# Kernel tuning notes

Measured on AMD Instinct MI355X. Metric: run time of the kernel, lower is better.

## Reference

```python
import jax, jax.numpy as jnp
import numpy as np

PATCH = 300
B, F = 16, 14
NOISE_FACTOR = 0.1
KERNEL = 7  # MedianPool2d(7, same=True) -> reflect pad 3 each side
PAD = 3
MED_IDX = (KERNEL * KERNEL - 1) // 2  # lower median of 49 = index 24


def median_pool7(x):
    """x: [C,H,W] -> [C,H,W], 7x7 median with reflect 'same' padding (MedianPool2d)."""
    C, H, W = x.shape
    xp = jnp.pad(x, ((0, 0), (PAD, PAD), (PAD, PAD)), mode='reflect')
    # 49 shifted views stacked on last axis: [C,H,W,49]
    wins = jnp.stack([xp[:, i:i + H, j:j + W]
                      for i in range(KERNEL) for j in range(KERNEL)], axis=-1)
    return jnp.sort(wins, axis=-1)[..., MED_IDX]


def setup_inputs() -> dict:
    key = jax.random.key(0)
    k1, k2, k3, k4, k5 = jax.random.split(key, 5)
    adv_patch = jax.random.uniform(k1, (3, PATCH, PATCH), dtype=jnp.float32)
    lab_batch = jax.random.uniform(k2, (B, F, 5), dtype=jnp.float32)
    contrast = jax.random.uniform(k3, (B, F), dtype=jnp.float32, minval=0.8, maxval=1.2)
    brightness = jax.random.uniform(k4, (B, F), dtype=jnp.float32, minval=-0.1, maxval=0.1)
    noise = jax.random.uniform(k5, (B, F, 3, PATCH, PATCH), dtype=jnp.float32, minval=-1.0, maxval=1.0)
    return {"adv_patch": adv_patch, "lab_batch": lab_batch, "contrast": contrast,
            "brightness": brightness, "noise": noise, "img_size": 416}


def reference(adv_patch, lab_batch, contrast, brightness, noise, img_size):
    # adv_patch side (300) <= img_size (416): interpolation branch skipped.
    p = median_pool7(adv_patch)                      # enable_blurred=True
    b, f = lab_batch.shape[0], lab_batch.shape[1]
    adv_batch = jnp.broadcast_to(p[None, None], (b, f) + p.shape)  # [B,F,3,P,P]
    c = contrast[:, :, None, None, None]
    br = brightness[:, :, None, None, None]
    adv_batch = adv_batch * c + br + noise * NOISE_FACTOR
    # with_black_trans=False branch
    return jnp.clip(adv_batch, 1e-6, 0.99999)
```

## Files before the change

kernel.cpp:

```cpp
#include <hip/hip_runtime.h>
#include <hip/hip_bf16.h>

#define PATCH    300
#define CHW      (PATCH*PATCH)
#define NPATCH   (3*CHW)
#define NSLAB    (16*14)
#define E8       (NPATCH/8)

#define FLAG_OFF 0
#define PMED_OFF 16

static __device__ __forceinline__ float bf2f(unsigned int bits16) {
    return __uint_as_float(bits16 << 16);
}

__global__ void detect_kernel(const unsigned short* __restrict__ patch,
                              int* __restrict__ flag) {
    int lane = threadIdx.x;
    unsigned int m = 0;
    for (int i = lane; i < 2048; i += 64) {
        unsigned int v = patch[i];
        m = m > v ? m : v;
    }
#pragma unroll
    for (int off = 32; off; off >>= 1) {
        unsigned int o = __shfl_down(m, off, 64);
        m = m > o ? m : o;
    }
    if (lane == 0) *flag = (m >= 0x8000u) ? 1 : 0;
}

#define CSWAP(x, y) do { float t_ = fminf(x, y); (y) = fmaxf(x, y); (x) = t_; } while (0)

template <bool F32>
static __device__ __forceinline__ float ldv(const void* pc, int off) {
    return F32 ? ((const float*)pc)[off]
               : bf2f(((const unsigned short*)pc)[off]);
}

template <bool F32>
static __device__ __forceinline__ float median49(const void* pc,
                                                 const int* ro, const int* ww) {
    float a[26];
#pragma unroll
    for (int k = 0; k < 26; ++k)
        a[k] = ldv<F32>(pc, ro[k / 7] + ww[k % 7]);

    float nxt = ldv<F32>(pc, ro[26 / 7] + ww[26 % 7]);
#pragma unroll
    for (int it = 0; it < 23; ++it) {
#pragma unroll
        for (int i = it + 1; i <= 25; ++i) CSWAP(a[it], a[i]);
#pragma unroll
        for (int i = it + 1; i < 25; ++i)  CSWAP(a[i], a[25]);
        a[25] = nxt;
        if (it < 22) {
            const int k = 27 + it;
            nxt = ldv<F32>(pc, ro[k / 7] + ww[k % 7]);
        }
    }
    float mn = fminf(a[23], a[24]);
    float mx = fmaxf(a[23], a[24]);
    return fmaxf(mn, fminf(mx, a[25]));
}

__global__ __launch_bounds__(256) void median7_kernel(
        const void* __restrict__ patchv,
        const int* __restrict__ flag,
        float* __restrict__ pmed) {
    int idx = blockIdx.x * 256 + threadIdx.x;
    if (idx >= NPATCH) return;
    int mode = *flag;
    int c   = idx / CHW;
    int rem = idx - c * CHW;
    int h   = rem / PATCH;
    int w   = rem - h * PATCH;

    int ro[7], ww[7];
#pragma unroll
    for (int d = 0; d < 7; d++) {
        int x = h + d - 3;
        x = x < 0 ? -x : (x >= PATCH ? 2 * PATCH - 2 - x : x);
        ro[d] = x * PATCH;
        int y = w + d - 3;
        ww[d] = y < 0 ? -y : (y >= PATCH ? 2 * PATCH - 2 - y : y);
    }

    float med;
    if (mode) {
        med = median49<true >((const void*)((const float*)patchv + c * CHW), ro, ww);
    } else {
        med = median49<false>((const void*)((const unsigned short*)patchv + c * CHW), ro, ww);
    }
    pmed[idx] = med;
}

__global__ __launch_bounds__(256) void apply_kernel(
        const float* __restrict__ pmed,
        const void* __restrict__ noisev,
        const void* __restrict__ contrastv,
        const void* __restrict__ brightnessv,
        const int* __restrict__ flag,
        float* __restrict__ out) {
    int slab = blockIdx.y;
    int g    = blockIdx.x * 256 + threadIdx.x;
    if (g >= E8) return;
    int mode = *flag;

    const float4* pm4 = (const float4*)pmed;
    float4 pa = pm4[2 * g], pb = pm4[2 * g + 1];
    float p[8] = {pa.x, pa.y, pa.z, pa.w, pb.x, pb.y, pb.z, pb.w};

    float c, br, n[8];
    if (mode) {
        c  = ((const float*)contrastv)[slab];
        br = ((const float*)brightnessv)[slab];
        const float4* n4 = (const float4*)noisev + (size_t)slab * (2 * E8);
        float4 na = n4[2 * g], nb = n4[2 * g + 1];
        n[0]=na.x; n[1]=na.y; n[2]=na.z; n[3]=na.w;
        n[4]=nb.x; n[5]=nb.y; n[6]=nb.z; n[7]=nb.w;
    } else {
        c  = bf2f(((const unsigned short*)contrastv)[slab]);
        br = bf2f(((const unsigned short*)brightnessv)[slab]);
        uint4 nv = ((const uint4*)noisev)[(size_t)slab * E8 + g];
        n[0]=bf2f(nv.x & 0xffffu); n[1]=bf2f(nv.x >> 16);
        n[2]=bf2f(nv.y & 0xffffu); n[3]=bf2f(nv.y >> 16);
        n[4]=bf2f(nv.z & 0xffffu); n[5]=bf2f(nv.z >> 16);
        n[6]=bf2f(nv.w & 0xffffu); n[7]=bf2f(nv.w >> 16);
    }

    float4 oa, ob;
    float r[8];
#pragma unroll
    for (int i = 0; i < 8; i++)
        r[i] = fminf(fmaxf(p[i] * c + br + n[i] * 0.1f, 1e-6f), 0.99999f);
    oa.x = r[0]; oa.y = r[1]; oa.z = r[2]; oa.w = r[3];
    ob.x = r[4]; ob.y = r[5]; ob.z = r[6]; ob.w = r[7];

    float4* o4 = (float4*)out + (size_t)slab * (2 * E8);
    o4[2 * g]     = oa;
    o4[2 * g + 1] = ob;
}

extern "C" void kernel_launch(void* const* d_in, const int* in_sizes, int n_in,
                              void* d_out, int out_size, void* d_ws, size_t ws_size,
                              hipStream_t stream) {
    const void* adv_patch  = d_in[0];
    const void* contrast   = d_in[2];
    const void* brightness = d_in[3];
    const void* noise      = d_in[4];

    int*   flag = (int*)((char*)d_ws + FLAG_OFF);
    float* pmed = (float*)((char*)d_ws + PMED_OFF);
    float* out  = (float*)d_out;

    detect_kernel<<<dim3(1), dim3(64), 0, stream>>>(
        (const unsigned short*)adv_patch, flag);

    median7_kernel<<<dim3((NPATCH + 255) / 256), dim3(256), 0, stream>>>(
        adv_patch, flag, pmed);

    dim3 g2((E8 + 255) / 256, NSLAB);
    apply_kernel<<<g2, dim3(256), 0, stream>>>(
        pmed, noise, contrast, brightness, flag, out);
}
```

Before: 428.6 us.

## Inline dtype detection into kernels and restructure apply loop for coalesced float4 access

Removes the separate single-wave detect kernel and the flag buffer, so each block instead detects f32 vs bf16 input from a wave-wide check of the first 1 KB of the patch. The apply kernel switches from 8 elements per thread in two adjacent float4 loads to four strided float4 loads per thread with a stride of 256, which gives fully coalesced accesses and more work per thread. This drops one launch and one dependency, but the detection heuristic now looks at fewer patch bytes and is repeated in every block.

```diff
diff --git a/kernel.cpp b/kernel.cpp
--- a/kernel.cpp
+++ b/kernel.cpp
@@ -1,33 +1,21 @@
 #include <hip/hip_runtime.h>
-#include <hip/hip_bf16.h>
 
 #define PATCH    300
 #define CHW      (PATCH*PATCH)
 #define NPATCH   (3*CHW)
 #define NSLAB    (16*14)
-#define E8       (NPATCH/8)
+#define NF4      (NPATCH/4)
 
-#define FLAG_OFF 0
-#define PMED_OFF 16
+#define PMED_OFF 0
 
 static __device__ __forceinline__ float bf2f(unsigned int bits16) {
     return __uint_as_float(bits16 << 16);
 }
 
-__global__ void detect_kernel(const unsigned short* __restrict__ patch,
-                              int* __restrict__ flag) {
-    int lane = threadIdx.x;
-    unsigned int m = 0;
-    for (int i = lane; i < 2048; i += 64) {
-        unsigned int v = patch[i];
-        m = m > v ? m : v;
-    }
-#pragma unroll
-    for (int off = 32; off; off >>= 1) {
-        unsigned int o = __shfl_down(m, off, 64);
-        m = m > o ? m : o;
-    }
-    if (lane == 0) *flag = (m >= 0x8000u) ? 1 : 0;
+static __device__ __forceinline__ int detect_f32(const void* patchv) {
+    const uint4* p4 = (const uint4*)patchv;
+    uint4 v = p4[threadIdx.x & 63];
+    return __any(((v.x | v.y | v.z | v.w) & 0x80008000u) != 0u);
 }
 
 #define CSWAP(x, y) do { float t_ = fminf(x, y); (y) = fmaxf(x, y); (x) = t_; } while (0)
@@ -66,11 +54,10 @@
 
 __global__ __launch_bounds__(256) void median7_kernel(
         const void* __restrict__ patchv,
-        const int* __restrict__ flag,
         float* __restrict__ pmed) {
+    int mode = detect_f32(patchv);
     int idx = blockIdx.x * 256 + threadIdx.x;
     if (idx >= NPATCH) return;
-    int mode = *flag;
     int c   = idx / CHW;
     int rem = idx - c * CHW;
     int h   = rem / PATCH;
@@ -95,51 +82,100 @@
     pmed[idx] = med;
 }
 
+#define CLIP1(p, n) fminf(fmaxf((p) * c + br + (n) * 0.1f, 1e-6f), 0.99999f)
+
 __global__ __launch_bounds__(256) void apply_kernel(
         const float* __restrict__ pmed,
+        const void* __restrict__ patchv,
         const void* __restrict__ noisev,
         const void* __restrict__ contrastv,
         const void* __restrict__ brightnessv,
-        const int* __restrict__ flag,
         float* __restrict__ out) {
+    int mode = detect_f32(patchv);
     int slab = blockIdx.y;
-    int g    = blockIdx.x * 256 + threadIdx.x;
-    if (g >= E8) return;
-    int mode = *flag;
+    int j0   = blockIdx.x * 1024 + threadIdx.x;
+    size_t s4 = (size_t)slab * NF4;
+    const float4* pm4 = (const float4*)pmed;
+    float4*       o4  = (float4*)out + s4;
 
-    const float4* pm4 = (const float4*)pmed;
-    float4 pa = pm4[2 * g], pb = pm4[2 * g + 1];
-    float p[8] = {pa.x, pa.y, pa.z, pa.w, pb.x, pb.y, pb.z, pb.w};
-
-    float c, br, n[8];
+    float c, br;
     if (mode) {
         c  = ((const float*)contrastv)[slab];
         br = ((const float*)brightnessv)[slab];
-        const float4* n4 = (const float4*)noisev + (size_t)slab * (2 * E8);
-        float4 na = n4[2 * g], nb = n4[2 * g + 1];
-        n[0]=na.x; n[1]=na.y; n[2]=na.z; n[3]=na.w;
-        n[4]=nb.x; n[5]=nb.y; n[6]=nb.z; n[7]=nb.w;
     } else {
         c  = bf2f(((const unsigned short*)contrastv)[slab]);
         br = bf2f(((const unsigned short*)brightnessv)[slab]);
-        uint4 nv = ((const uint4*)noisev)[(size_t)slab * E8 + g];
-        n[0]=bf2f(nv.x & 0xffffu); n[1]=bf2f(nv.x >> 16);
-        n[2]=bf2f(nv.y & 0xffffu); n[3]=bf2f(nv.y >> 16);
-        n[4]=bf2f(nv.z & 0xffffu); n[5]=bf2f(nv.z >> 16);
-        n[6]=bf2f(nv.w & 0xffffu); n[7]=bf2f(nv.w >> 16);
     }
 
-    float4 oa, ob;
-    float r[8];
+    bool full = (j0 + 3 * 256) < NF4;
+
+    if (mode) {
+        const float4* n4 = (const float4*)noisev + s4;
+        if (full) {
+            float4 p[4], n[4];
 #pragma unroll
-    for (int i = 0; i < 8; i++)
-        r[i] = fminf(fmaxf(p[i] * c + br + n[i] * 0.1f, 1e-6f), 0.99999f);
-    oa.x = r[0]; oa.y = r[1]; oa.z = r[2]; oa.w = r[3];
-    ob.x = r[4]; ob.y = r[5]; ob.z = r[6]; ob.w = r[7];
-
-    float4* o4 = (float4*)out + (size_t)slab * (2 * E8);
-    o4[2 * g]     = oa;
-    o4[2 * g + 1] = ob;
+            for (int k = 0; k < 4; ++k) p[k] = pm4[j0 + k * 256];
+#pragma unroll
+            for (int k = 0; k < 4; ++k) n[k] = n4[j0 + k * 256];
+#pragma unroll
+            for (int k = 0; k < 4; ++k) {
+                float4 r;
+                r.x = CLIP1(p[k].x, n[k].x);
+                r.y = CLIP1(p[k].y, n[k].y);
+                r.z = CLIP1(p[k].z, n[k].z);
+                r.w = CLIP1(p[k].w, n[k].w);
+                o4[j0 + k * 256] = r;
+            }
+        } else {
+#pragma unroll
+            for (int k = 0; k < 4; ++k) {
+                int j = j0 + k * 256;
+                if (j < NF4) {
+                    float4 p = pm4[j], n = n4[j];
+                    float4 r;
+                    r.x = CLIP1(p.x, n.x);
+                    r.y = CLIP1(p.y, n.y);
+                    r.z = CLIP1(p.z, n.z);
+                    r.w = CLIP1(p.w, n.w);
+                    o4[j] = r;
+                }
+            }
+        }
+    } else {
+        const uint2* n2 = (const uint2*)noisev + s4;
+        if (full) {
+            float4 p[4];
+            uint2  nv[4];
+#pragma unroll
+            for (int k = 0; k < 4; ++k) p[k]  = pm4[j0 + k * 256];
+#pragma unroll
+            for (int k = 0; k < 4; ++k) nv[k] = n2[j0 + k * 256];
+#pragma unroll
+            for (int k = 0; k < 4; ++k) {
+                float4 r;
+                r.x = CLIP1(p[k].x, bf2f(nv[k].x & 0xffffu));
+                r.y = CLIP1(p[k].y, bf2f(nv[k].x >> 16));
+                r.z = CLIP1(p[k].z, bf2f(nv[k].y & 0xffffu));
+                r.w = CLIP1(p[k].w, bf2f(nv[k].y >> 16));
+                o4[j0 + k * 256] = r;
+            }
+        } else {
+#pragma unroll
+            for (int k = 0; k < 4; ++k) {
+                int j = j0 + k * 256;
+                if (j < NF4) {
+                    float4 p  = pm4[j];
+                    uint2  nv = n2[j];
+                    float4 r;
+                    r.x = CLIP1(p.x, bf2f(nv.x & 0xffffu));
+                    r.y = CLIP1(p.y, bf2f(nv.x >> 16));
+                    r.z = CLIP1(p.z, bf2f(nv.y & 0xffffu));
+                    r.w = CLIP1(p.w, bf2f(nv.y >> 16));
+                    o4[j] = r;
+                }
+            }
+        }
+    }
 }
 
 extern "C" void kernel_launch(void* const* d_in, const int* in_sizes, int n_in,
@@ -150,17 +186,13 @@
     const void* brightness = d_in[3];
     const void* noise      = d_in[4];
 
-    int*   flag = (int*)((char*)d_ws + FLAG_OFF);
     float* pmed = (float*)((char*)d_ws + PMED_OFF);
     float* out  = (float*)d_out;
 
-    detect_kernel<<<dim3(1), dim3(64), 0, stream>>>(
-        (const unsigned short*)adv_patch, flag);
+    median7_kernel<<<dim3((NPATCH + 255) / 256), dim3(256), 0, stream>>>(
+        adv_patch, pmed);
 
-    median7_kernel<<<dim3((NPATCH + 255) / 256), dim3(256), 0, stream>>>(
-        adv_patch, flag, pmed);
-
-    dim3 g2((E8 + 255) / 256, NSLAB);
+    dim3 g2((NF4 + 1023) / 1024, NSLAB);
     apply_kernel<<<g2, dim3(256), 0, stream>>>(
-        pmed, noise, contrast, brightness, flag, out);
+        pmed, adv_patch, noise, contrast, brightness, out);
 }
```

Measured after the change: 417.0 us. 1.03x faster.
